# Optimization experiments

Measured on AMD Instinct MI355X. Metric: run time of the kernel, lower is better.

The kernel has to match this reference:

```python
import jax, jax.numpy as jnp
import numpy as np

NUM_HEADS = 6

def setup_inputs() -> dict:
    key = jax.random.key(0)
    k1, k2, k3, k4 = jax.random.split(key, 4)
    B, N, C = 8, 2048, 384
    x = jax.random.normal(k1, (B, N, C), dtype=jnp.float32)
    qkv_w = jax.random.normal(k2, (3 * C, C), dtype=jnp.float32) * (C ** -0.5)
    proj_w = jax.random.normal(k3, (C, C), dtype=jnp.float32) * (C ** -0.5)
    proj_b = jax.random.normal(k4, (C,), dtype=jnp.float32) * 0.01
    temperature = jnp.ones((NUM_HEADS, 1, 1), dtype=jnp.float32)
    return {"x": x, "qkv_w": qkv_w, "proj_w": proj_w, "proj_b": proj_b,
            "temperature": temperature}


def reference(x, qkv_w, proj_w, proj_b, temperature):
    B, N, C = x.shape
    H = NUM_HEADS
    Dh = C // H
    # qkv projection (no bias), split into q, k, v per head
    qkv = (x @ qkv_w.T).reshape(B, N, 3, H, Dh)
    qkv = jnp.transpose(qkv, (2, 0, 3, 1, 4))  # [3, B, H, N, Dh]
    q, k, v = qkv[0], qkv[1], qkv[2]
    # scores scaled by sqrt(C) (full dim, as in source), then learnable temperature
    attn = jnp.einsum('bhnd,bhmd->bhnm', q, k) / (C ** 0.5)
    attn = attn / temperature  # temperature: [H,1,1] broadcasts over B and N,N
    # diagonal (self-token) mask -> -inf before softmax
    diag = jnp.eye(N, dtype=bool)
    attn = jnp.where(diag, -jnp.inf, attn)
    attn = jax.nn.softmax(attn, axis=-1)
    # attend and merge heads
    out = jnp.einsum('bhnm,bhmd->bhnd', attn, v)
    out = jnp.transpose(out, (0, 2, 1, 3)).reshape(B, N, C)
    # output projection
    return out @ proj_w.T + proj_b
```

## Files before the change

### kernel.cpp

```cpp
#include <hip/hip_runtime.h>


using f32x4 = __attribute__((ext_vector_type(4))) float;
using s16x8 = __attribute__((ext_vector_type(8))) short;
using u16x4 = __attribute__((ext_vector_type(4))) unsigned short;
using u32x2 = __attribute__((ext_vector_type(2))) unsigned int;
typedef unsigned short u16;
typedef unsigned int u32;

#define MFMA16(a, b, c) __builtin_amdgcn_mfma_f32_16x16x32_bf16(a, b, c, 0, 0, 0)
#define LOG2E 1.4426950408889634f
#define SQRTC 19.595917942265423f

__device__ __forceinline__ u16 f2bf(float f) {
  u32 u = __float_as_uint(f);
  u += 0x7fffu + ((u >> 16) & 1u);
  return (u16)(u >> 16);
}

__device__ __forceinline__ u32 cvtpk(float lo, float hi) {
  u32 r;
  asm("v_cvt_pk_bf16_f32 %0, %1, %2" : "=v"(r) : "v"(lo), "v"(hi));
  return r;
}

__device__ __forceinline__ float fexp2(float x) {
  float r;
  asm("v_exp_f32 %0, %1" : "=v"(r) : "v"(x));
  return r;
}

__device__ __forceinline__ void gld16(const void* g, void* l) {
  __builtin_amdgcn_global_load_lds((const __attribute__((address_space(1))) void*)g,
                                   (__attribute__((address_space(3))) void*)l, 16, 0, 0);
}

__global__ __launch_bounds__(256) void k_cvt(const float* __restrict__ in,
                                             u16* __restrict__ out) {
  const size_t i = (size_t)blockIdx.x * 256 + threadIdx.x;
  f32x4 v = *(const f32x4*)(in + i * 4);
  u16x4 o;
  o[0] = f2bf(v[0]); o[1] = f2bf(v[1]); o[2] = f2bf(v[2]); o[3] = f2bf(v[3]);
  *(u16x4*)(out + i * 4) = o;
}

__global__ __launch_bounds__(256) void k_qkv(const u16* __restrict__ X,
                                             const u16* __restrict__ W,
                                             const float* __restrict__ temp,
                                             u16* __restrict__ Qb,
                                             u16* __restrict__ Kb,
                                             u16* __restrict__ Vt) {
  __shared__ u16 As[2][128 * 32];
  __shared__ u16 Bs[2][128 * 32];
  const int tid = threadIdx.x, w = tid >> 6, l = tid & 63, lr = l & 15, lg = l >> 4;
  const int tn = blockIdx.x * 128, tm = blockIdx.y * 128;
  const int wr = w >> 1, wc = w & 1;
  const int r0 = tid >> 2, c8 = (tid & 3) * 8;

  f32x4 acc[4][4] = {};

  auto stage = [&](int buf, int kt) {
    const int k0 = kt * 32;
    char* da = (char*)(&As[buf][0]) + (w << 10);
    char* db = (char*)(&Bs[buf][0]) + (w << 10);
    gld16(X + (size_t)(tm + r0) * 384 + k0 + c8, da);
    gld16(X + (size_t)(tm + 64 + r0) * 384 + k0 + c8, da + 4096);
    gld16(W + (size_t)(tn + r0) * 384 + k0 + c8, db);
    gld16(W + (size_t)(tn + 64 + r0) * 384 + k0 + c8, db + 4096);
  };

  stage(0, 0);
  for (int kt = 0; kt < 12; ++kt) {
    __syncthreads();
    if (kt < 11) stage((kt + 1) & 1, kt + 1);
    const int buf = kt & 1;
    s16x8 af[4], bfr[4];
    for (int mi = 0; mi < 4; mi++)
      af[mi] = *(const s16x8*)&As[buf][(wr * 64 + mi * 16 + lr) * 32 + lg * 8];
    for (int ni = 0; ni < 4; ni++)
      bfr[ni] = *(const s16x8*)&Bs[buf][(wc * 64 + ni * 16 + lr) * 32 + lg * 8];
    for (int mi = 0; mi < 4; mi++)
      for (int ni = 0; ni < 4; ni++)
        acc[mi][ni] = MFMA16(af[mi], bfr[ni], acc[mi][ni]);
  }

  for (int mi = 0; mi < 4; mi++)
    for (int ni = 0; ni < 4; ni++) {
      const int n = tn + wc * 64 + ni * 16 + lr;
      const int which = n / 384;
      const int c = n - which * 384;
      const int h = c >> 6, d = c & 63;
      const float mult = (which == 0) ? (LOG2E / (SQRTC * temp[h])) : 1.0f;
      for (int j = 0; j < 4; j++) {
        const int m = tm + wr * 64 + mi * 16 + lg * 4 + j;
        const int b = m >> 11, pos = m & 2047;
        const u16 val = f2bf(acc[mi][ni][j] * mult);
        const size_t bh = (size_t)(b * 6 + h);
        if (which == 0)      Qb[(bh * 2048 + pos) * 64 + d] = val;
        else if (which == 1) Kb[(bh * 2048 + pos) * 64 + d] = val;
        else                 Vt[(bh * 64 + d) * 2048 + pos] = val;
      }
    }
}

#define LDSOFF(row, c16) (((row) * 128 + (c16) * 16) ^ (((row) & 7) << 4))

__global__ __launch_bounds__(256, 3) void k_attn(const u16* __restrict__ Qb,
                                                 const u16* __restrict__ Kb,
                                                 const u16* __restrict__ Vt,
                                                 u16* __restrict__ AO) {
  __shared__ u16 Ks[2][64 * 64];
  __shared__ u16 Vs[2][64 * 64];
  __shared__ u16 Ps[4][32 * 72];
  const int tid = threadIdx.x, w = tid >> 6, l = tid & 63, lr = l & 15, lg = l >> 4;
  const int orig = blockIdx.x;
  const int rm = (orig & 7) * 96 + (orig >> 3);
  const int qt = rm & 15, bh = rm >> 4;
  const int h = bh % 6, b = bh / 6;
  const size_t base = (size_t)bh << 17;
  const int q0 = qt * 128 + w * 32;
  const int maskKt = q0 >> 6;
  const int qo = q0 & 63;

  s16x8 qf[2][2];
  for (int mi = 0; mi < 2; mi++)
    for (int ks = 0; ks < 2; ks++)
      qf[mi][ks] = *(const s16x8*)&Qb[base + (size_t)(q0 + mi * 16 + lr) * 64 + ks * 32 + lg * 8];

  s16x8 ones;
  for (int e = 0; e < 8; ++e) ones[e] = (short)0x3F80;

  f32x4 o0[4] = {}, o1[4] = {};
  f32x4 os0 = {}, os1 = {};

  const int r0 = tid >> 3, c0 = tid & 7;
  const int c8 = c0 * 8;
  const int wo0 = LDSOFF(r0, c0), wo1 = LDSOFF(r0 + 32, c0);

  s16x8 ka0, ka1, va0, va1;
  auto issue = [&](int kt) {
    const u16* kp = Kb + base + (size_t)(kt * 64 + r0) * 64 + c8;
    ka0 = *(const s16x8*)kp;
    ka1 = *(const s16x8*)(kp + 32 * 64);
    const u16* vp = Vt + base + (size_t)r0 * 2048 + kt * 64 + c8;
    va0 = *(const s16x8*)vp;
    va1 = *(const s16x8*)(vp + 32 * 2048);
  };
  auto commit = [&](int buf) {
    char* kd = (char*)&Ks[buf][0];
    char* vd = (char*)&Vs[buf][0];
    *(s16x8*)(kd + wo0) = ka0; *(s16x8*)(kd + wo1) = ka1;
    *(s16x8*)(vd + wo0) = va0; *(s16x8*)(vd + wo1) = va1;
  };

  issue(0); commit(0);
  __syncthreads();

  const int lrs = (lr & 7) << 4;
  const int x0 = (lg * 16) ^ lrs;
  const int x1 = (64 + lg * 16) ^ lrs;

  for (int kt = 0; kt < 32; ++kt) {
    const int cur = kt & 1;
    if (kt < 31) issue(kt + 1);

    f32x4 st0[4] = {}, st1[4] = {};
    const char* kbp = (const char*)&Ks[cur][0];
    __builtin_amdgcn_s_setprio(1);
    for (int ni = 0; ni < 4; ++ni) {
      const int rb = (ni * 16 + lr) * 128;
      const s16x8 kf0 = *(const s16x8*)(kbp + (rb + x0));
      const s16x8 kf1 = *(const s16x8*)(kbp + (rb + x1));
      st0[ni] = MFMA16(kf0, qf[0][0], st0[ni]);
      st0[ni] = MFMA16(kf1, qf[0][1], st0[ni]);
      st1[ni] = MFMA16(kf0, qf[1][0], st1[ni]);
      st1[ni] = MFMA16(kf1, qf[1][1], st1[ni]);
    }
    __builtin_amdgcn_s_setprio(0);

    if (kt == maskKt) {
      for (int ni = 0; ni < 4; ++ni)
        for (int j = 0; j < 4; ++j) {
          const int kvl = ni * 16 + lg * 4 + j;
          if (kvl == qo + lr)      st0[ni][j] = -1e30f;
          if (kvl == qo + 16 + lr) st1[ni][j] = -1e30f;
        }
    }

    u16* const psw = &Ps[w][0];
    {
      u16* pr = psw + lr * 72 + lg * 4;
      for (int ni = 0; ni < 4; ++ni) {
        u32x2 d2;
        d2[0] = cvtpk(fexp2(st0[ni][0]), fexp2(st0[ni][1]));
        d2[1] = cvtpk(fexp2(st0[ni][2]), fexp2(st0[ni][3]));
        *(u32x2*)(pr + ni * 16) = d2;
      }
      pr = psw + (16 + lr) * 72 + lg * 4;
      for (int ni = 0; ni < 4; ++ni) {
        u32x2 d2;
        d2[0] = cvtpk(fexp2(st1[ni][0]), fexp2(st1[ni][1]));
        d2[1] = cvtpk(fexp2(st1[ni][2]), fexp2(st1[ni][3]));
        *(u32x2*)(pr + ni * 16) = d2;
      }
    }

    const char* vbp = (const char*)&Vs[cur][0];
    __builtin_amdgcn_s_setprio(1);
    for (int ks = 0; ks < 2; ++ks) {
      const s16x8 pa0 = *(const s16x8*)((const char*)(psw + lr * 72) + ks * 64 + lg * 16);
      const s16x8 pa1 = *(const s16x8*)((const char*)(psw + (16 + lr) * 72) + ks * 64 + lg * 16);
      const int xk = ks ? x1 : x0;
      for (int dj = 0; dj < 4; ++dj) {
        const s16x8 vf = *(const s16x8*)(vbp + ((dj * 16 + lr) * 128 + xk));
        o0[dj] = MFMA16(pa0, vf, o0[dj]);
        o1[dj] = MFMA16(pa1, vf, o1[dj]);
      }
      os0 = MFMA16(pa0, ones, os0);
      os1 = MFMA16(pa1, ones, os1);
    }
    __builtin_amdgcn_s_setprio(0);

    if (kt < 31) commit(cur ^ 1);
    __syncthreads();
  }

  f32x4 rv0, rv1;
  for (int j = 0; j < 4; ++j) { rv0[j] = 1.0f / os0[j]; rv1[j] = 1.0f / os1[j]; }
  const size_t aobase = (size_t)b * 2048 * 384 + (size_t)h * 64;
  for (int j = 0; j < 4; ++j) {
    const int pos0 = q0 + lg * 4 + j;
    const int pos1 = pos0 + 16;
    for (int dj = 0; dj < 4; ++dj) {
      AO[aobase + (size_t)pos0 * 384 + dj * 16 + lr] = f2bf(o0[dj][j] * rv0[j]);
      AO[aobase + (size_t)pos1 * 384 + dj * 16 + lr] = f2bf(o1[dj][j] * rv1[j]);
    }
  }
}

__global__ __launch_bounds__(256) void k_proj(const u16* __restrict__ A,
                                              const u16* __restrict__ W,
                                              const float* __restrict__ bias,
                                              float* __restrict__ out) {
  __shared__ u16 As[2][128 * 32];
  __shared__ u16 Bs[2][128 * 32];
  const int tid = threadIdx.x, w = tid >> 6, l = tid & 63, lr = l & 15, lg = l >> 4;
  const int tn = blockIdx.x * 128, tm = blockIdx.y * 128;
  const int wr = w >> 1, wc = w & 1;
  const int r0 = tid >> 2, c8 = (tid & 3) * 8;

  f32x4 acc[4][4] = {};

  auto stage = [&](int buf, int kt) {
    const int k0 = kt * 32;
    char* da = (char*)(&As[buf][0]) + (w << 10);
    char* db = (char*)(&Bs[buf][0]) + (w << 10);
    gld16(A + (size_t)(tm + r0) * 384 + k0 + c8, da);
    gld16(A + (size_t)(tm + 64 + r0) * 384 + k0 + c8, da + 4096);
    gld16(W + (size_t)(tn + r0) * 384 + k0 + c8, db);
    gld16(W + (size_t)(tn + 64 + r0) * 384 + k0 + c8, db + 4096);
  };

  stage(0, 0);
  for (int kt = 0; kt < 12; ++kt) {
    __syncthreads();
    if (kt < 11) stage((kt + 1) & 1, kt + 1);
    const int buf = kt & 1;
    s16x8 af[4], bfr[4];
    for (int mi = 0; mi < 4; mi++)
      af[mi] = *(const s16x8*)&As[buf][(wr * 64 + mi * 16 + lr) * 32 + lg * 8];
    for (int ni = 0; ni < 4; ni++)
      bfr[ni] = *(const s16x8*)&Bs[buf][(wc * 64 + ni * 16 + lr) * 32 + lg * 8];
    for (int mi = 0; mi < 4; mi++)
      for (int ni = 0; ni < 4; ni++)
        acc[mi][ni] = MFMA16(af[mi], bfr[ni], acc[mi][ni]);
  }

  for (int mi = 0; mi < 4; mi++)
    for (int ni = 0; ni < 4; ni++) {
      const int n = tn + wc * 64 + ni * 16 + lr;
      const float bn = bias[n];
      for (int j = 0; j < 4; j++) {
        const int m = tm + wr * 64 + mi * 16 + lg * 4 + j;
        out[(size_t)m * 384 + n] = acc[mi][ni][j] + bn;
      }
    }
}

extern "C" void kernel_launch(void* const* d_in, const int* in_sizes, int n_in,
                              void* d_out, int out_size, void* d_ws, size_t ws_size,
                              hipStream_t stream) {
  const float* x      = (const float*)d_in[0];
  const float* qkv_w  = (const float*)d_in[1];
  const float* proj_w = (const float*)d_in[2];
  const float* proj_b = (const float*)d_in[3];
  const float* temp   = (const float*)d_in[4];
  float* out = (float*)d_out;

  u16* xb     = (u16*)d_ws;
  u16* wqkvb  = xb + 6291456;
  u16* wprojb = wqkvb + 442368;
  u16* Qb     = wprojb + 147456;
  u16* Kb     = Qb + 6291456;
  u16* Vtb    = Kb + 6291456;
  u16* AOb    = Vtb + 6291456;

  k_cvt<<<6144, 256, 0, stream>>>(x, xb);
  k_cvt<<<432, 256, 0, stream>>>(qkv_w, wqkvb);
  k_cvt<<<144, 256, 0, stream>>>(proj_w, wprojb);
  k_qkv<<<dim3(9, 128), 256, 0, stream>>>(xb, wqkvb, temp, Qb, Kb, Vtb);
  k_attn<<<768, 256, 0, stream>>>(Qb, Kb, Vtb, AOb);
  k_proj<<<dim3(3, 128), 256, 0, stream>>>(AOb, wprojb, proj_b, out);
}
```

Before: 137.2 us.

## Fuse x fp32-to-bf16 conversion into QKV GEMM, vectorize V stores, reorder attention PV

```diff
diff --git a/kernel.cpp b/kernel.cpp
--- a/kernel.cpp
+++ b/kernel.cpp
@@ -5,6 +5,7 @@
 using s16x8 = __attribute__((ext_vector_type(8))) short;
 using u16x4 = __attribute__((ext_vector_type(4))) unsigned short;
 using u32x2 = __attribute__((ext_vector_type(2))) unsigned int;
+using u32x4 = __attribute__((ext_vector_type(4))) unsigned int;
 typedef unsigned short u16;
 typedef unsigned int u32;
 
@@ -44,7 +45,7 @@
   *(u16x4*)(out + i * 4) = o;
 }
 
-__global__ __launch_bounds__(256) void k_qkv(const u16* __restrict__ X,
+__global__ __launch_bounds__(256) void k_qkv(const float* __restrict__ X,
                                              const u16* __restrict__ W,
                                              const float* __restrict__ temp,
                                              u16* __restrict__ Qb,
@@ -56,23 +57,38 @@
   const int tn = blockIdx.x * 128, tm = blockIdx.y * 128;
   const int wr = w >> 1, wc = w & 1;
   const int r0 = tid >> 2, c8 = (tid & 3) * 8;
+  const int ar = tid >> 1, ac = (tid & 1) * 16;
 
   f32x4 acc[4][4] = {};
-
-  auto stage = [&](int buf, int kt) {
+  f32x4 a4[4];
+
+  auto issueA = [&](int kt) {
+    const float* xp = X + (size_t)(tm + ar) * 384 + kt * 32 + ac;
+    a4[0] = *(const f32x4*)(xp);
+    a4[1] = *(const f32x4*)(xp + 4);
+    a4[2] = *(const f32x4*)(xp + 8);
+    a4[3] = *(const f32x4*)(xp + 12);
+  };
+  auto commitA = [&](int buf) {
+    u32x4 h0, h1;
+    h0[0] = cvtpk(a4[0][0], a4[0][1]); h0[1] = cvtpk(a4[0][2], a4[0][3]);
+    h0[2] = cvtpk(a4[1][0], a4[1][1]); h0[3] = cvtpk(a4[1][2], a4[1][3]);
+    h1[0] = cvtpk(a4[2][0], a4[2][1]); h1[1] = cvtpk(a4[2][2], a4[2][3]);
+    h1[2] = cvtpk(a4[3][0], a4[3][1]); h1[3] = cvtpk(a4[3][2], a4[3][3]);
+    *(u32x4*)&As[buf][ar * 32 + ac] = h0;
+    *(u32x4*)&As[buf][ar * 32 + ac + 8] = h1;
+  };
+  auto stageB = [&](int buf, int kt) {
     const int k0 = kt * 32;
-    char* da = (char*)(&As[buf][0]) + (w << 10);
     char* db = (char*)(&Bs[buf][0]) + (w << 10);
-    gld16(X + (size_t)(tm + r0) * 384 + k0 + c8, da);
-    gld16(X + (size_t)(tm + 64 + r0) * 384 + k0 + c8, da + 4096);
     gld16(W + (size_t)(tn + r0) * 384 + k0 + c8, db);
     gld16(W + (size_t)(tn + 64 + r0) * 384 + k0 + c8, db + 4096);
   };
 
-  stage(0, 0);
+  issueA(0); stageB(0, 0); commitA(0);
   for (int kt = 0; kt < 12; ++kt) {
     __syncthreads();
-    if (kt < 11) stage((kt + 1) & 1, kt + 1);
+    if (kt < 11) { issueA(kt + 1); stageB((kt + 1) & 1, kt + 1); }
     const int buf = kt & 1;
     s16x8 af[4], bfr[4];
     for (int mi = 0; mi < 4; mi++)
@@ -82,23 +98,31 @@
     for (int mi = 0; mi < 4; mi++)
       for (int ni = 0; ni < 4; ni++)
         acc[mi][ni] = MFMA16(af[mi], bfr[ni], acc[mi][ni]);
+    if (kt < 11) commitA((kt + 1) & 1);
   }
 
+  const int which = (tn + wc * 64) / 384;
+  const int bidx = (tm >> 11);
   for (int mi = 0; mi < 4; mi++)
     for (int ni = 0; ni < 4; ni++) {
       const int n = tn + wc * 64 + ni * 16 + lr;
-      const int which = n / 384;
       const int c = n - which * 384;
       const int h = c >> 6, d = c & 63;
-      const float mult = (which == 0) ? (LOG2E / (SQRTC * temp[h])) : 1.0f;
-      for (int j = 0; j < 4; j++) {
-        const int m = tm + wr * 64 + mi * 16 + lg * 4 + j;
-        const int b = m >> 11, pos = m & 2047;
-        const u16 val = f2bf(acc[mi][ni][j] * mult);
-        const size_t bh = (size_t)(b * 6 + h);
-        if (which == 0)      Qb[(bh * 2048 + pos) * 64 + d] = val;
-        else if (which == 1) Kb[(bh * 2048 + pos) * 64 + d] = val;
-        else                 Vt[(bh * 64 + d) * 2048 + pos] = val;
+      const size_t bh = (size_t)(bidx * 6 + h);
+      if (which == 2) {
+        const int pos0 = (tm + wr * 64 + mi * 16 + lg * 4) & 2047;
+        u16x4 vv;
+        vv[0] = f2bf(acc[mi][ni][0]); vv[1] = f2bf(acc[mi][ni][1]);
+        vv[2] = f2bf(acc[mi][ni][2]); vv[3] = f2bf(acc[mi][ni][3]);
+        *(u16x4*)&Vt[(bh * 64 + d) * 2048 + pos0] = vv;
+      } else {
+        const float mult = (which == 0) ? (LOG2E / (SQRTC * temp[h])) : 1.0f;
+        for (int j = 0; j < 4; j++) {
+          const int pos = (tm + wr * 64 + mi * 16 + lg * 4 + j) & 2047;
+          const u16 val = f2bf(acc[mi][ni][j] * mult);
+          if (which == 0) Qb[(bh * 2048 + pos) * 64 + d] = val;
+          else            Kb[(bh * 2048 + pos) * 64 + d] = val;
+        }
       }
     }
 }
@@ -187,6 +211,14 @@
         }
     }
 
+    const char* vbp = (const char*)&Vs[cur][0];
+    s16x8 vfr[2][4];
+    for (int ks = 0; ks < 2; ++ks) {
+      const int xk = ks ? x1 : x0;
+      for (int dj = 0; dj < 4; ++dj)
+        vfr[ks][dj] = *(const s16x8*)(vbp + ((dj * 16 + lr) * 128 + xk));
+    }
+
     u16* const psw = &Ps[w][0];
     {
       u16* pr = psw + lr * 72 + lg * 4;
@@ -196,7 +228,19 @@
         d2[1] = cvtpk(fexp2(st0[ni][2]), fexp2(st0[ni][3]));
         *(u32x2*)(pr + ni * 16) = d2;
       }
-      pr = psw + (16 + lr) * 72 + lg * 4;
+    }
+    {
+      const s16x8 pa0k0 = *(const s16x8*)((const char*)(psw + lr * 72) + 0 * 64 + lg * 16);
+      const s16x8 pa0k1 = *(const s16x8*)((const char*)(psw + lr * 72) + 1 * 64 + lg * 16);
+      __builtin_amdgcn_s_setprio(1);
+      for (int dj = 0; dj < 4; ++dj) o0[dj] = MFMA16(pa0k0, vfr[0][dj], o0[dj]);
+      os0 = MFMA16(pa0k0, ones, os0);
+      for (int dj = 0; dj < 4; ++dj) o0[dj] = MFMA16(pa0k1, vfr[1][dj], o0[dj]);
+      os0 = MFMA16(pa0k1, ones, os0);
+      __builtin_amdgcn_s_setprio(0);
+    }
+    {
+      u16* pr = psw + (16 + lr) * 72 + lg * 4;
       for (int ni = 0; ni < 4; ++ni) {
         u32x2 d2;
         d2[0] = cvtpk(fexp2(st1[ni][0]), fexp2(st1[ni][1]));
@@ -204,22 +248,16 @@
         *(u32x2*)(pr + ni * 16) = d2;
       }
     }
-
-    const char* vbp = (const char*)&Vs[cur][0];
-    __builtin_amdgcn_s_setprio(1);
-    for (int ks = 0; ks < 2; ++ks) {
-      const s16x8 pa0 = *(const s16x8*)((const char*)(psw + lr * 72) + ks * 64 + lg * 16);
-      const s16x8 pa1 = *(const s16x8*)((const char*)(psw + (16 + lr) * 72) + ks * 64 + lg * 16);
-      const int xk = ks ? x1 : x0;
-      for (int dj = 0; dj < 4; ++dj) {
-        const s16x8 vf = *(const s16x8*)(vbp + ((dj * 16 + lr) * 128 + xk));
-        o0[dj] = MFMA16(pa0, vf, o0[dj]);
-        o1[dj] = MFMA16(pa1, vf, o1[dj]);
-      }
-      os0 = MFMA16(pa0, ones, os0);
-      os1 = MFMA16(pa1, ones, os1);
-    }
-    __builtin_amdgcn_s_setprio(0);
+    {
+      const s16x8 pa1k0 = *(const s16x8*)((const char*)(psw + (16 + lr) * 72) + 0 * 64 + lg * 16);
+      const s16x8 pa1k1 = *(const s16x8*)((const char*)(psw + (16 + lr) * 72) + 1 * 64 + lg * 16);
+      __builtin_amdgcn_s_setprio(1);
+      for (int dj = 0; dj < 4; ++dj) o1[dj] = MFMA16(pa1k0, vfr[0][dj], o1[dj]);
+      os1 = MFMA16(pa1k0, ones, os1);
+      for (int dj = 0; dj < 4; ++dj) o1[dj] = MFMA16(pa1k1, vfr[1][dj], o1[dj]);
+      os1 = MFMA16(pa1k1, ones, os1);
+      __builtin_amdgcn_s_setprio(0);
+    }
 
     if (kt < 31) commit(cur ^ 1);
     __syncthreads();
@@ -297,18 +335,16 @@
   const float* temp   = (const float*)d_in[4];
   float* out = (float*)d_out;
 
-  u16* xb     = (u16*)d_ws;
-  u16* wqkvb  = xb + 6291456;
+  u16* wqkvb  = (u16*)d_ws;
   u16* wprojb = wqkvb + 442368;
   u16* Qb     = wprojb + 147456;
   u16* Kb     = Qb + 6291456;
   u16* Vtb    = Kb + 6291456;
   u16* AOb    = Vtb + 6291456;
 
-  k_cvt<<<6144, 256, 0, stream>>>(x, xb);
   k_cvt<<<432, 256, 0, stream>>>(qkv_w, wqkvb);
   k_cvt<<<144, 256, 0, stream>>>(proj_w, wprojb);
-  k_qkv<<<dim3(9, 128), 256, 0, stream>>>(xb, wqkvb, temp, Qb, Kb, Vtb);
+  k_qkv<<<dim3(9, 128), 256, 0, stream>>>(x, wqkvb, temp, Qb, Kb, Vtb);
   k_attn<<<768, 256, 0, stream>>>(Qb, Kb, Vtb, AOb);
   k_proj<<<dim3(3, 128), 256, 0, stream>>>(AOb, wprojb, proj_b, out);
 }
```

After: 133.3 us. -2.9%, faster.
